# Performance work log

Hardware: AMD Instinct MI355X
Metric: run time of the kernel (lower is better)

Reference implementation:

```python
import jax, jax.numpy as jnp
import numpy as np

MODES = (16, 16, 16)  # (kx, ky, kz); rfft keeps kz//2+1 = 9 modes on last axis


def setup_inputs() -> dict:
    key = jax.random.key(0)
    k_x, k_w1, k_w2 = jax.random.split(key, 3)
    B, C, H, W, D = 4, 64, 64, 64, 64
    hidden = C // 4
    kzr = MODES[2] // 2 + 1
    gate_dim = MODES[0] * MODES[1] * kzr  # 16*16*9 = 2304
    x = jax.random.normal(k_x, (B, C, H, W, D), dtype=jnp.float32)
    w1 = jax.random.normal(k_w1, (C, hidden), dtype=jnp.float32) * (1.0 / np.sqrt(C))
    b1 = jnp.zeros((hidden,), dtype=jnp.float32)
    w2 = jax.random.normal(k_w2, (hidden, gate_dim), dtype=jnp.float32) * (1.0 / np.sqrt(hidden))
    b2 = jnp.zeros((gate_dim,), dtype=jnp.float32)
    return {"x": x, "w1": w1, "b1": b1, "w2": w2, "b2": b2}


def reference(x, w1, b1, w2, b2):
    B = x.shape[0]
    kx, ky, kz = MODES
    kzr = kz // 2 + 1
    # Gate network: global average pool over spatial dims -> MLP -> sigmoid
    pooled = jnp.mean(x, axis=(2, 3, 4))                      # [B, C]
    h = jax.nn.relu(pooled @ w1 + b1)                          # [B, C//4]
    gates = jax.nn.sigmoid(h @ w2 + b2)                        # [B, kx*ky*kzr]
    gates = gates.reshape(B, 1, kx, ky, kzr)                   # broadcast over channels
    # Full 3D rFFT, gate only the low-frequency corner block, inverse FFT
    x_ft = jnp.fft.rfftn(x, axes=(-3, -2, -1))                 # [B, C, H, W, D//2+1] complex
    x_ft_gated = x_ft.at[:, :, :kx, :ky, :kzr].multiply(gates.astype(x_ft.real.dtype))
    out = jnp.fft.irfftn(x_ft_gated, s=x.shape[-3:], axes=(-3, -2, -1))
    return out.astype(x.dtype)
```

## Files before the change

### kernel.cpp

```cpp
#include <hip/hip_runtime.h>

namespace {

constexpr float COS64[64] = {
  1.00000000f,  0.99518473f,  0.98078528f,  0.95694034f,
  0.92387953f,  0.88192126f,  0.83146961f,  0.77301045f,
  0.70710678f,  0.63439328f,  0.55557023f,  0.47139674f,
  0.38268343f,  0.29028468f,  0.19509032f,  0.09801714f,
  0.00000000f, -0.09801714f, -0.19509032f, -0.29028468f,
 -0.38268343f, -0.47139674f, -0.55557023f, -0.63439328f,
 -0.70710678f, -0.77301045f, -0.83146961f, -0.88192126f,
 -0.92387953f, -0.95694034f, -0.98078528f, -0.99518473f,
 -1.00000000f, -0.99518473f, -0.98078528f, -0.95694034f,
 -0.92387953f, -0.88192126f, -0.83146961f, -0.77301045f,
 -0.70710678f, -0.63439328f, -0.55557023f, -0.47139674f,
 -0.38268343f, -0.29028468f, -0.19509032f, -0.09801714f,
 -0.00000000f,  0.09801714f,  0.19509032f,  0.29028468f,
  0.38268343f,  0.47139674f,  0.55557023f,  0.63439328f,
  0.70710678f,  0.77301045f,  0.83146961f,  0.88192126f,
  0.92387953f,  0.95694034f,  0.98078528f,  0.99518473f };

constexpr float TWOPI_64 = 0.09817477042468103f;
constexpr int MM = 144;
constexpr int GD = 2304;

__device__ __forceinline__ void rot_mi(int m, float r_in, float i_in,
                                       float& r_out, float& i_out) {
  float r  = (m & 1) ? i_in : r_in;
  float i2 = (m & 1) ? r_in : i_in;
  r  = (m >= 2) ? -r : r;
  i2 = (m == 1 || m == 2) ? -i2 : i2;
  r_out = r; i_out = i2;
}

__global__ __launch_bounds__(256) void k1_fwd(const float* __restrict__ x,
                                              float2* __restrict__ buf1) {
  __shared__ float xs[64 * 68];
  __shared__ float2 As[9 * 67];
  const int tid = threadIdx.x;
  const int slice = blockIdx.x;
  const int w = tid >> 2, q = tid & 3;

  const float4* xp = (const float4*)(x + ((size_t)slice << 12));
  const float4 a0 = xp[tid];
  const float4 a1 = xp[tid + 256];
  const float4 a2 = xp[tid + 512];
  const float4 a3 = xp[tid + 768];
  {
    const int s0 = tid & 15, hi = tid >> 4;
    *(float4*)&xs[(hi +  0) * 68 + s0 * 4] = a0;
    *(float4*)&xs[(hi + 16) * 68 + s0 * 4] = a1;
    *(float4*)&xs[(hi + 32) * 68 + s0 * 4] = a2;
    *(float4*)&xs[(hi + 48) * 68 + s0 * 4] = a3;
  }
  __syncthreads();

  float xv[16];
  {
    const float4 b0 = *(const float4*)&xs[w * 68 + q * 16 + 0];
    const float4 b1 = *(const float4*)&xs[w * 68 + q * 16 + 4];
    const float4 b2 = *(const float4*)&xs[w * 68 + q * 16 + 8];
    const float4 b3 = *(const float4*)&xs[w * 68 + q * 16 + 12];
    xv[0]=b0.x; xv[1]=b0.y; xv[2]=b0.z; xv[3]=b0.w;
    xv[4]=b1.x; xv[5]=b1.y; xv[6]=b1.z; xv[7]=b1.w;
    xv[8]=b2.x; xv[9]=b2.y; xv[10]=b2.z; xv[11]=b2.w;
    xv[12]=b3.x; xv[13]=b3.y; xv[14]=b3.z; xv[15]=b3.w;
  }

  float ar[9], ai[9];
#pragma unroll
  for (int kz = 0; kz < 9; ++kz) { ar[kz] = 0.f; ai[kz] = 0.f; }
#pragma unroll
  for (int j = 0; j < 16; ++j) {
    const float v = xv[j];
#pragma unroll
    for (int kz = 0; kz < 9; ++kz) {
      const int n = (kz * j) & 63;
      ar[kz] = fmaf(v, COS64[n], ar[kz]);
      ai[kz] = fmaf(v, -COS64[(n + 48) & 63], ai[kz]);
    }
  }
#pragma unroll
  for (int kz = 0; kz < 9; ++kz) {
    const int m = (q * kz) & 3;
    float r, i2;
    rot_mi(m, ar[kz], ai[kz], r, i2);
    r  += __shfl_xor(r, 1);  r  += __shfl_xor(r, 2);
    i2 += __shfl_xor(i2, 1); i2 += __shfl_xor(i2, 2);
    if (q == 0) As[kz * 67 + w] = make_float2(r, i2);
  }
  __syncthreads();

  if (tid < MM) {
    const int ky = tid / 9, kz = tid - ky * 9;
    const float cs = COS64[ky], sn = COS64[(ky + 48) & 63];
    const int m1 = ky & 3, m2 = (2 * ky) & 3, m3 = (3 * ky) & 3;
    float px = 1.f, py = 0.f, br = 0.f, bi = 0.f;
    const float2* Ak = As + kz * 67;
#pragma unroll
    for (int b = 0; b < 16; ++b) {
      const float2 v0 = Ak[b];
      const float2 v1 = Ak[b + 16];
      const float2 v2 = Ak[b + 32];
      const float2 v3 = Ak[b + 48];
      float gr = v0.x, gi = v0.y, rr, ri;
      rot_mi(m1, v1.x, v1.y, rr, ri); gr += rr; gi += ri;
      rot_mi(m2, v2.x, v2.y, rr, ri); gr += rr; gi += ri;
      rot_mi(m3, v3.x, v3.y, rr, ri); gr += rr; gi += ri;
      br = fmaf(gr, px, fmaf(-gi, py, br));
      bi = fmaf(gr, py, fmaf( gi, px, bi));
      const float nx = fmaf(px, cs,  py * sn);
      const float ny = fmaf(py, cs, -px * sn);
      px = nx; py = ny;
    }
    buf1[(size_t)slice * MM + tid] = make_float2(br, bi);
  }
}

__global__ __launch_bounds__(256) void k2_fwd(const float2* __restrict__ buf1,
                                              float2* __restrict__ buf2) {
  __shared__ float2 Bs[32 * MM];
  const int tid = threadIdx.x, bc = blockIdx.x;
  const int kx = tid >> 4, g = tid & 15;

  float accR[9], accI[9];
#pragma unroll
  for (int j = 0; j < 9; ++j) { accR[j] = 0.f; accI[j] = 0.f; }
  float qR = 1.f, qI = 0.f;
  const float hc = COS64[kx], hsn = COS64[(kx + 48) & 63];

  const float4* src = (const float4*)(buf1 + (size_t)bc * 64 * MM);
  for (int c2 = 0; c2 < 2; ++c2) {
    float4* dst4 = (float4*)Bs;
    for (int i = tid; i < 2304; i += 256) dst4[i] = src[c2 * 2304 + i];
    __syncthreads();
    for (int hh = 0; hh < 32; ++hh) {
      const float2* row = Bs + hh * MM + g * 9;
#pragma unroll
      for (int j = 0; j < 9; ++j) {
        const float2 b = row[j];
        accR[j] = fmaf(b.x, qR, fmaf(-b.y, qI, accR[j]));
        accI[j] = fmaf(b.x, qI, fmaf( b.y, qR, accI[j]));
      }
      const float nR = fmaf(qR, hc, qI * hsn);
      const float nI = fmaf(qI, hc, -qR * hsn);
      qR = nR; qI = nI;
    }
    __syncthreads();
  }

  float2* dst = buf2 + (size_t)bc * GD + kx * MM + g * 9;
#pragma unroll
  for (int j = 0; j < 9; ++j) dst[j] = make_float2(accR[j], accI[j]);
}

__global__ __launch_bounds__(256) void k3_gates(const float2* __restrict__ buf2,
    const float* __restrict__ w1, const float* __restrict__ b1,
    const float* __restrict__ w2, const float* __restrict__ b2,
    float* __restrict__ gm1) {
  __shared__ float pooled[64];
  __shared__ float hs[16];
  const int b = blockIdx.x, tid = threadIdx.x;
  if (tid < 64)
    pooled[tid] = buf2[(size_t)(b * 64 + tid) * GD].x * (1.f / 262144.f);
  __syncthreads();
  if (tid < 16) {
    float acc = b1[tid];
    for (int c = 0; c < 64; ++c) acc = fmaf(pooled[c], w1[c * 16 + tid], acc);
    hs[tid] = fmaxf(acc, 0.f);
  }
  __syncthreads();
#pragma unroll
  for (int r = 0; r < 9; ++r) {
    const int o = tid + r * 256;
    float acc = b2[o];
#pragma unroll
    for (int j = 0; j < 16; ++j) acc = fmaf(hs[j], w2[j * GD + o], acc);
    gm1[b * GD + o] = 1.f / (1.f + expf(-acc)) - 1.f;
  }
}

__global__ __launch_bounds__(256) void k4b_final(const float2* __restrict__ S,
                                                 const float* __restrict__ gm1,
                                                 const float* __restrict__ x,
                                                 float* __restrict__ out) {
  __shared__ float2 C1s[MM];
  __shared__ float2 C2s[9 * 65];
  __shared__ float deltaS[64 * 68];
  const int tid = threadIdx.x;
  const int slice = 16383 - blockIdx.x;
  const int bc = slice >> 6, h = slice & 63, b = bc >> 6;
  const int w = tid >> 2, q = tid & 3;

  const float4* xp = (const float4*)(x + ((size_t)slice << 12));
  const float4 xv0 = xp[tid];
  const float4 xv1 = xp[tid + 256];
  const float4 xv2 = xp[tid + 512];
  const float4 xv3 = xp[tid + 768];

  if (tid < MM) {
    const float2* Sp = S + (size_t)bc * GD + tid;
    const float* Gp = gm1 + (size_t)b * GD + tid;
    float sn, cs;
    sincosf(TWOPI_64 * (float)h, &sn, &cs);
    float px = 1.f, py = 0.f, ar = 0.f, ai = 0.f;
#pragma unroll
    for (int kx = 0; kx < 16; ++kx) {
      const float2 sv = Sp[kx * MM];
      const float g = Gp[kx * MM];
      const float dR = sv.x * g, dI = sv.y * g;
      ar = fmaf(dR, px, fmaf(-dI, py, ar));
      ai = fmaf(dR, py, fmaf( dI, px, ai));
      const float nx = fmaf(px, cs, -py * sn);
      const float ny = fmaf(px, sn,  py * cs);
      px = nx; py = ny;
    }
    C1s[tid] = make_float2(ar, ai);
  }
  __syncthreads();

  {
    float sn, cs;
    sincosf(TWOPI_64 * (float)w, &sn, &cs);
    const int kz0 = q, kz1 = q + 4;
    float a0r = 0.f, a0i = 0.f, a1r = 0.f, a1i = 0.f, a2r = 0.f, a2i = 0.f;
    float px = 1.f, py = 0.f;
    for (int ky = 0; ky < 16; ++ky) {
      const float2 c0 = C1s[ky * 9 + kz0];
      const float2 c1 = C1s[ky * 9 + kz1];
      a0r = fmaf(c0.x, px, fmaf(-c0.y, py, a0r));
      a0i = fmaf(c0.x, py, fmaf( c0.y, px, a0i));
      a1r = fmaf(c1.x, px, fmaf(-c1.y, py, a1r));
      a1i = fmaf(c1.x, py, fmaf( c1.y, px, a1i));
      if (q == 0) {
        const float2 c2v = C1s[ky * 9 + 8];
        a2r = fmaf(c2v.x, px, fmaf(-c2v.y, py, a2r));
        a2i = fmaf(c2v.x, py, fmaf( c2v.y, px, a2i));
      }
      const float nx = fmaf(px, cs, -py * sn);
      const float ny = fmaf(px, sn,  py * cs);
      px = nx; py = ny;
    }
    C2s[kz0 * 65 + w] = make_float2(a0r, a0i);
    C2s[kz1 * 65 + w] = make_float2(a1r, a1i);
    if (q == 0) C2s[8 * 65 + w] = make_float2(a2r, a2i);
  }
  __syncthreads();

  {
    float cr[9], ci[9];
#pragma unroll
    for (int kz = 0; kz < 9; ++kz) {
      const float2 v = C2s[kz * 65 + w];
      const int m = (kz * q) & 3;
      const float a = v.x, b2_ = v.y;
      float r  = (m & 1) ? b2_ : a;
      float i2 = (m & 1) ? a : b2_;
      r  = (m == 1 || m == 2) ? -r : r;
      i2 = (m >= 2) ? -i2 : i2;
      cr[kz] = r; ci[kz] = i2;
    }
    float acc[16];
#pragma unroll
    for (int j = 0; j < 16; ++j) acc[j] = cr[0];
#pragma unroll
    for (int kz = 1; kz < 9; ++kz) {
#pragma unroll
      for (int j = 0; j < 16; ++j) {
        const int n = (kz * j) & 63;
        acc[j] = fmaf(cr[kz],  2.f * COS64[n], acc[j]);
        acc[j] = fmaf(ci[kz], -2.f * COS64[(n + 48) & 63], acc[j]);
      }
    }
    const float scale = 1.f / 262144.f;
    float4 d0, d1, d2, d3;
    d0.x = acc[0]  * scale; d0.y = acc[1]  * scale;
    d0.z = acc[2]  * scale; d0.w = acc[3]  * scale;
    d1.x = acc[4]  * scale; d1.y = acc[5]  * scale;
    d1.z = acc[6]  * scale; d1.w = acc[7]  * scale;
    d2.x = acc[8]  * scale; d2.y = acc[9]  * scale;
    d2.z = acc[10] * scale; d2.w = acc[11] * scale;
    d3.x = acc[12] * scale; d3.y = acc[13] * scale;
    d3.z = acc[14] * scale; d3.w = acc[15] * scale;
    *(float4*)&deltaS[w * 68 + q * 16 + 0]  = d0;
    *(float4*)&deltaS[w * 68 + q * 16 + 4]  = d1;
    *(float4*)&deltaS[w * 68 + q * 16 + 8]  = d2;
    *(float4*)&deltaS[w * 68 + q * 16 + 12] = d3;
  }
  __syncthreads();

  {
    const int s0 = tid & 15, hi = tid >> 4;
    const float4 r0 = *(const float4*)&deltaS[(hi +  0) * 68 + s0 * 4];
    const float4 r1 = *(const float4*)&deltaS[(hi + 16) * 68 + s0 * 4];
    const float4 r2 = *(const float4*)&deltaS[(hi + 32) * 68 + s0 * 4];
    const float4 r3 = *(const float4*)&deltaS[(hi + 48) * 68 + s0 * 4];
    float4* op = (float4*)(out + ((size_t)slice << 12));
    float4 o0 = xv0, o1 = xv1, o2 = xv2, o3 = xv3;
    o0.x += r0.x; o0.y += r0.y; o0.z += r0.z; o0.w += r0.w;
    o1.x += r1.x; o1.y += r1.y; o1.z += r1.z; o1.w += r1.w;
    o2.x += r2.x; o2.y += r2.y; o2.z += r2.z; o2.w += r2.w;
    o3.x += r3.x; o3.y += r3.y; o3.z += r3.z; o3.w += r3.w;
    op[tid]       = o0;
    op[tid + 256] = o1;
    op[tid + 512] = o2;
    op[tid + 768] = o3;
  }
}

}

extern "C" void kernel_launch(void* const* d_in, const int* in_sizes, int n_in,
                              void* d_out, int out_size, void* d_ws, size_t ws_size,
                              hipStream_t stream) {
  (void)in_sizes; (void)n_in; (void)out_size; (void)ws_size;
  const float* x  = (const float*)d_in[0];
  const float* w1 = (const float*)d_in[1];
  const float* b1 = (const float*)d_in[2];
  const float* w2 = (const float*)d_in[3];
  const float* b2 = (const float*)d_in[4];
  float* out = (float*)d_out;

  char* ws = (char*)d_ws;
  float2* buf1 = (float2*)ws;
  float2* buf2 = (float2*)(ws + 18874368);
  float*  gm1  = (float*)(ws + 18874368 + 4718592);

  hipLaunchKernelGGL(k1_fwd,   dim3(16384),    dim3(256), 0, stream, x, buf1);
  hipLaunchKernelGGL(k2_fwd,   dim3(256),      dim3(256), 0, stream, buf1, buf2);
  hipLaunchKernelGGL(k3_gates, dim3(4),        dim3(256), 0, stream, buf2, w1, b1, w2, b2, gm1);
  hipLaunchKernelGGL(k4b_final,dim3(16384),    dim3(256), 0, stream, buf2, gm1, x, out);
}
```

Before: 237.7 us.

## Split inverse kx-transform into separate kernel computing C1 for all slices

Moves the per-slice inverse DFT over kx (gated spectrum times twiddles) out of the final kernel into a new kernel with one block per (b,c). That block stages the gated spectrum once in shared memory and computes C1 for all 64 h rows using a twiddle table instead of sincos and recurrence. The final kernel then only loads a precomputed 144-entry C1 row. This removes 64x redundant global reads of S and gm1 and per-slice serial work, at the cost of an extra launch and a 9.4MB intermediate buffer round trip.

```diff
diff --git a/kernel.cpp b/kernel.cpp
--- a/kernel.cpp
+++ b/kernel.cpp
@@ -180,8 +180,48 @@
   }
 }
 
-__global__ __launch_bounds__(256) void k4b_final(const float2* __restrict__ S,
-                                                 const float* __restrict__ gm1,
+__global__ __launch_bounds__(256) void k4a_c1(const float2* __restrict__ S,
+                                              const float* __restrict__ gm1,
+                                              float2* __restrict__ C1buf) {
+  __shared__ float2 Dg[GD];
+  __shared__ float2 rotS[64 * 16];
+  const int tid = threadIdx.x, bc = blockIdx.x, b = bc >> 6;
+
+  for (int i = tid; i < GD; i += 256) {
+    const float2 sv = S[(size_t)bc * GD + i];
+    const float g = gm1[(size_t)b * GD + i];
+    Dg[i] = make_float2(sv.x * g, sv.y * g);
+  }
+#pragma unroll
+  for (int u = 0; u < 4; ++u) {
+    const int e = tid * 4 + u, hh = e >> 4, kx = e & 15;
+    const int n = (kx * hh) & 63;
+    rotS[e] = make_float2(COS64[n], COS64[(n + 48) & 63]);
+  }
+  __syncthreads();
+
+  const int h = tid >> 2, mq = tid & 3;
+  float2* dst = C1buf + ((size_t)(bc * 64 + h)) * MM + mq * 36;
+  for (int jb = 0; jb < 3; ++jb) {
+    float aR[12], aI[12];
+#pragma unroll
+    for (int j = 0; j < 12; ++j) { aR[j] = 0.f; aI[j] = 0.f; }
+    for (int kx = 0; kx < 16; ++kx) {
+      const float2 rot = rotS[h * 16 + kx];
+      const float2* drow = Dg + kx * MM + mq * 36 + jb * 12;
+#pragma unroll
+      for (int j = 0; j < 12; ++j) {
+        const float2 d = drow[j];
+        aR[j] = fmaf(d.x, rot.x, fmaf(-d.y, rot.y, aR[j]));
+        aI[j] = fmaf(d.x, rot.y, fmaf( d.y, rot.x, aI[j]));
+      }
+    }
+#pragma unroll
+    for (int j = 0; j < 12; ++j) dst[jb * 12 + j] = make_float2(aR[j], aI[j]);
+  }
+}
+
+__global__ __launch_bounds__(256) void k4b_final(const float2* __restrict__ C1buf,
                                                  const float* __restrict__ x,
                                                  float* __restrict__ out) {
   __shared__ float2 C1s[MM];
@@ -189,7 +229,6 @@
   __shared__ float deltaS[64 * 68];
   const int tid = threadIdx.x;
   const int slice = 16383 - blockIdx.x;
-  const int bc = slice >> 6, h = slice & 63, b = bc >> 6;
   const int w = tid >> 2, q = tid & 3;
 
   const float4* xp = (const float4*)(x + ((size_t)slice << 12));
@@ -198,24 +237,9 @@
   const float4 xv2 = xp[tid + 512];
   const float4 xv3 = xp[tid + 768];
 
-  if (tid < MM) {
-    const float2* Sp = S + (size_t)bc * GD + tid;
-    const float* Gp = gm1 + (size_t)b * GD + tid;
-    float sn, cs;
-    sincosf(TWOPI_64 * (float)h, &sn, &cs);
-    float px = 1.f, py = 0.f, ar = 0.f, ai = 0.f;
-#pragma unroll
-    for (int kx = 0; kx < 16; ++kx) {
-      const float2 sv = Sp[kx * MM];
-      const float g = Gp[kx * MM];
-      const float dR = sv.x * g, dI = sv.y * g;
-      ar = fmaf(dR, px, fmaf(-dI, py, ar));
-      ai = fmaf(dR, py, fmaf( dI, px, ai));
-      const float nx = fmaf(px, cs, -py * sn);
-      const float ny = fmaf(px, sn,  py * cs);
-      px = nx; py = ny;
-    }
-    C1s[tid] = make_float2(ar, ai);
+  if (tid < 72) {
+    const float4* cp = (const float4*)(C1buf + (size_t)slice * MM);
+    ((float4*)C1s)[tid] = cp[tid];
   }
   __syncthreads();
 
@@ -322,12 +346,14 @@
   float* out = (float*)d_out;
 
   char* ws = (char*)d_ws;
-  float2* buf1 = (float2*)ws;
-  float2* buf2 = (float2*)(ws + 18874368);
-  float*  gm1  = (float*)(ws + 18874368 + 4718592);
+  float2* buf1  = (float2*)ws;
+  float2* buf2  = (float2*)(ws + 18874368);
+  float*  gm1   = (float*)(ws + 23592960);
+  float2* c1buf = (float2*)(ws + 23629824);
 
   hipLaunchKernelGGL(k1_fwd,   dim3(16384),    dim3(256), 0, stream, x, buf1);
   hipLaunchKernelGGL(k2_fwd,   dim3(256),      dim3(256), 0, stream, buf1, buf2);
   hipLaunchKernelGGL(k3_gates, dim3(4),        dim3(256), 0, stream, buf2, w1, b1, w2, b2, gm1);
-  hipLaunchKernelGGL(k4b_final,dim3(16384),    dim3(256), 0, stream, buf2, gm1, x, out);
-}
+  hipLaunchKernelGGL(k4a_c1,   dim3(256),      dim3(256), 0, stream, buf2, gm1, c1buf);
+  hipLaunchKernelGGL(k4b_final,dim3(16384),    dim3(256), 0, stream, c1buf, x, out);
+}
```

Result: no change. 234.6 us (-1.3%).
